# Kernel optimization log

Measured on AMD Instinct MI355X. Metric: run time of the kernel, lower is better.

The kernel has to match this reference:

```python
import jax, jax.numpy as jnp
import numpy as np

LAGRANGE_ORDER = 5  # fixed, as in the torch module


def _lagrange_weights(alpha):
    """Vectorised Lagrange weights of length L+1. alpha: [B,N] -> [B,N,L+1]."""
    L = LAGRANGE_ORDER
    j = jnp.arange(L + 1, dtype=alpha.dtype)
    u = alpha[..., None] - j                          # [B,N,L+1]
    denom = j[:, None] - j[None, :]                   # [L+1,L+1]
    mask = ~jnp.eye(L + 1, dtype=bool)
    num = jnp.where(mask, u[..., None, :], jnp.ones_like(u)[..., None, :])
    den = jnp.where(mask, denom, jnp.ones_like(denom))
    return (num / den).prod(axis=-1)                  # [B,N,L+1]


def setup_inputs() -> dict:
    key = jax.random.key(0)
    k1, k2, k3 = jax.random.split(key, 3)
    B, N = 16, 16384
    # fractional period in samples, in [40, 100) -> max floor(f0)=99, K=99+5+3=107<=108
    f0 = 40.0 + 60.0 * jax.random.uniform(k1, (B, N), dtype=jnp.float32)
    x = jax.random.normal(k2, (B, N), dtype=jnp.float32)
    l_b = jax.random.uniform(k3, (B, N, 2), dtype=jnp.float32)  # (g, p) in [0,1]
    return {"f0": f0, "x": x, "l_b": l_b, "K": 108}


def reference(f0, x, l_b, K):
    B, N = x.shape
    L = LAGRANGE_ORDER
    # design_loop: (g, p) -> loop taps [b0, a1]; gain capped <1 for stability
    g = 0.99 * l_b[..., 0]
    p = l_b[..., 1]
    b0 = g * (1.0 - p)                                # [B,N]
    a1 = g * p
    # tune_f0: subtract low-frequency phase delay of (b0 + a1 z^-1)
    f0c = f0 - a1 / (b0 + a1 + 1e-7)
    # Lagrange centre & weights
    z = jnp.floor(f0c).astype(jnp.int32)
    z_center = z - L // 2                             # [B,N]
    alpha = f0c - z_center.astype(f0.dtype)
    w = _lagrange_weights(alpha)                      # [B,N,L+1]
    # compute_resonator_matrix: loop filter convolved with fractional delay -> block [B,N,L+2]
    block = (b0[..., None] * jnp.pad(w, ((0, 0), (0, 0), (0, 1)))
             + a1[..., None] * jnp.pad(w, ((0, 0), (0, 0), (1, 0))))
    # scatter (-block) into A; LPC lag k+1 lives in column k
    cols = z_center[..., None] - 1 + jnp.arange(L + 2)  # [B,N,L+2]
    cols = jnp.clip(cols, 0, K - 1)
    A = jnp.zeros((B, N, K), x.dtype).at[
        jnp.arange(B)[:, None, None], jnp.arange(N)[None, :, None], cols
    ].add(-block)
    # sample_wise_lpc: y[n] = x[n] - sum_k A[n,k] * y[n-1-k], zero init state
    def step(buf, inp):
        a_n, x_n = inp                                 # [B,K], [B]
        y_n = x_n - jnp.sum(a_n * buf, axis=-1)
        buf = jnp.concatenate([y_n[:, None], buf[:, :-1]], axis=1)
        return buf, y_n
    buf0 = jnp.zeros((B, K), x.dtype)
    _, ys = jax.lax.scan(step, buf0, (A.transpose(1, 0, 2), x.T))  # ys: [N,B]
    return ys.T
```

## Files before the change

### kernel.cpp

```cpp
#include <hip/hip_runtime.h>
#include <math.h>


#define B_    16
#define N_    16384
#define S_    16
#define NSEG  1024
#define NITER 28
#define RUNS  104
#define CHUNK 37
#define HROWS 263
#define ZROW0 150

#define TG_FLOATS (B_ * S_ * RUNS * RUNS)
#define ST_FLOATS (B_ * S_ * RUNS)

__device__ __forceinline__ void diffks_coeffs(float f0v, float lbg, float lbp,
                                              int n, float4& lo, float4& hi) {
  float g  = 0.99f * lbg;
  float p  = lbp;
  float b0 = g * (1.0f - p);
  float a1 = g * p;
  float f0c = f0v - a1 / (b0 + a1 + 1e-7f);
  int   zc  = (int)floorf(f0c) - 2;
  float alpha = f0c - (float)zc;
  float u0 = alpha;
  float u1 = alpha - 1.0f;
  float u2 = alpha - 2.0f;
  float u3 = alpha - 3.0f;
  float u4 = alpha - 4.0f;
  float u5 = alpha - 5.0f;
  float w0 = u1 * u2 * u3 * u4 * u5 * (-1.0f / 120.0f);
  float w1 = u0 * u2 * u3 * u4 * u5 * ( 1.0f /  24.0f);
  float w2 = u0 * u1 * u3 * u4 * u5 * (-1.0f /  12.0f);
  float w3 = u0 * u1 * u2 * u4 * u5 * ( 1.0f /  12.0f);
  float w4 = u0 * u1 * u2 * u3 * u5 * (-1.0f /  24.0f);
  float w5 = u0 * u1 * u2 * u3 * u4 * ( 1.0f / 120.0f);
  lo.x = b0 * w0;
  lo.y = fmaf(b0, w1, a1 * w0);
  lo.z = fmaf(b0, w2, a1 * w1);
  lo.w = fmaf(b0, w3, a1 * w2);
  hi.x = fmaf(b0, w4, a1 * w3);
  hi.y = fmaf(b0, w5, a1 * w4);
  hi.z = a1 * w5;
  hi.w = __int_as_float((n - 6 - zc) & 255);
}

__global__ __launch_bounds__(1024) void diffks_phase1(
    const float* __restrict__ f0, const float* __restrict__ lb,
    const float* __restrict__ x, float* __restrict__ Tg) {
  const int bs = blockIdx.x;
  const int b  = bs >> 4, s = bs & 15;
  const int n0 = s << 10;
  const int tid = threadIdx.x;

  __shared__ __align__(16) float hist[HROWS * RUNS];
  __shared__ float4 sLo[NSEG], sHi[NSEG];
  __shared__ float  sX[NSEG];

  {
    const size_t gi = (size_t)b * N_ + n0 + tid;
    const float2 lv = ((const float2*)lb)[gi];
    float4 lo, hi;
    diffks_coeffs(f0[gi], lv.x, lv.y, tid, lo, hi);
    sLo[tid] = lo; sHi[tid] = hi; sX[tid] = x[gi];
  }
  {
    float4* __restrict__ hz = (float4*)(hist + ZROW0 * RUNS);
    const int nz = ((HROWS - ZROW0) * RUNS) / 4;
    for (int i = tid; i < nz; i += 1024)
      hz[i] = float4{0.0f, 0.0f, 0.0f, 0.0f};
  }
  __syncthreads();
  if (tid < 103) hist[(255 - tid) * RUNS + tid] = 1.0f;
  __syncthreads();

  {
    const int w    = tid >> 6;
    const int lane = tid & 63;
    const int cl   = 2 * lane;
    const bool act = (lane < 52);
    const bool px  = (lane == 51);
    float* __restrict__ hcol = hist + cl;

    for (int t = 0; t < 32; ++t) {
#pragma unroll
      for (int u = 0; u < 2; ++u) {
        const int p = 32 * t + 2 * w + u;
        const float4 lo = sLo[p];
        const float4 hi = sHi[p];
        const float  xv = sX[p];
        if (act) {
          const int base = __float_as_int(hi.w);
          const float* __restrict__ hr = hcol + base * RUNS;
          float2 acc;
          acc.x = 0.0f;
          acc.y = px ? xv : 0.0f;
          const float c[7] = {hi.z, hi.y, hi.x, lo.w, lo.z, lo.y, lo.x};
#pragma unroll
          for (int m = 0; m < 7; ++m) {
            const float2 v = *(const float2*)(hr + m * RUNS);
            acc.x = fmaf(c[m], v.x, acc.x);
            acc.y = fmaf(c[m], v.y, acc.y);
          }
          const int wsl = p & 255;
          *(float2*)(hcol + wsl * RUNS) = acc;
          if (wsl < 7)
            *(float2*)(hcol + (wsl + 256) * RUNS) = acc;
        }
      }
      __syncthreads();
    }
  }

  float* __restrict__ T = Tg + (size_t)bs * RUNS * RUNS;
  for (int idx = tid; idx < RUNS * RUNS; idx += 1024) {
    const int r = idx / RUNS;
    const int j = idx - r * RUNS;
    T[idx] = (j < 103) ? hist[((255 - j) & 255) * RUNS + r] : 0.0f;
  }
}

#define P2_STEP(s_, tv_)                                                      \
  {                                                                           \
    if (q == 0) states[((size_t)b * S_ + (s_)) * RUNS + j] = cur[j];          \
    float acc = 0.0f;                                                         \
    _Pragma("unroll")                                                         \
    for (int k = 0; k < 13; ++k) acc = fmaf(tv_[k], cur[r0 + k], acc);        \
    if ((s_) + 2 < S_) {                                                      \
      const float* __restrict__ Tn = Tb + (size_t)((s_) + 2) * RUNS * RUNS;   \
      _Pragma("unroll")                                                       \
      for (int k = 0; k < 13; ++k) tv_[k] = Tn[(size_t)(r0 + k) * RUNS + j];  \
    }                                                                         \
    part[q][j] = acc;                                                         \
    __syncthreads();                                                          \
    if (q == 0) {                                                             \
      float v = 0.0f;                                                         \
      _Pragma("unroll")                                                       \
      for (int qq = 0; qq < 8; ++qq) v += part[qq][j];                        \
      cur[j] = (j < 103) ? v : 1.0f;                                          \
    }                                                                         \
    __syncthreads();                                                          \
  }

__global__ __launch_bounds__(832) void diffks_phase2(
    const float* __restrict__ Tg, float* __restrict__ states) {
  const int b   = blockIdx.x;
  const int tid = threadIdx.x;
  const int j   = tid % RUNS;
  const int q   = tid / RUNS;
  const int r0  = 13 * q;
  __shared__ float cur[RUNS];
  __shared__ float part[8][105];
  if (tid < 103) cur[tid] = 0.0f;
  if (tid == 103) cur[103] = 1.0f;
  __syncthreads();

  const float* __restrict__ Tb = Tg + (size_t)b * S_ * RUNS * RUNS;
  float tvA[13], tvB[13];
#pragma unroll
  for (int k = 0; k < 13; ++k)
    tvA[k] = Tb[(size_t)(r0 + k) * RUNS + j];
#pragma unroll
  for (int k = 0; k < 13; ++k)
    tvB[k] = Tb[(size_t)RUNS * RUNS + (size_t)(r0 + k) * RUNS + j];

#pragma unroll
  for (int sp = 0; sp < 8; ++sp) {
    P2_STEP(2 * sp,     tvA)
    P2_STEP(2 * sp + 1, tvB)
  }
}

__global__ __launch_bounds__(256) void diffks_phase3(
    const float* __restrict__ f0, const float* __restrict__ lb,
    const float* __restrict__ x, const float* __restrict__ states,
    float* __restrict__ y) {
  const int bs = blockIdx.x;
  const int b  = bs >> 4, s = bs & 15;
  const int n0 = s << 10;
  const int tid = threadIdx.x;

  __shared__ __align__(16) float ring[512];
  __shared__ float4 sC[2 * NSEG];
  __shared__ float  sX[NSEG];
  __shared__ float  sY[NSEG];

#pragma unroll
  for (int k = 0; k < 2; ++k) ring[tid + 256 * k] = 0.0f;
  {
    const size_t gb = (size_t)b * N_ + n0;
    const float*  __restrict__ f0b = f0 + gb;
    const float2* __restrict__ lbb = (const float2*)(lb + 2 * gb);
    const float*  __restrict__ xb  = x + gb;
    float  vf[4]; float2 vl[4]; float vx[4];
#pragma unroll
    for (int k = 0; k < 4; ++k) {
      const int i = tid + 256 * k;
      vf[k] = f0b[i]; vl[k] = lbb[i]; vx[k] = xb[i];
    }
#pragma unroll
    for (int k = 0; k < 4; ++k) {
      const int i = tid + 256 * k;
      float4 lo, hi;
      diffks_coeffs(vf[k], vl[k].x, vl[k].y, n0 + i, lo, hi);
      sC[2 * i] = lo; sC[2 * i + 1] = hi; sX[i] = vx[k];
    }
  }
  __syncthreads();
  const float* __restrict__ st = states + (size_t)bs * RUNS;
  if (tid < 103) {
    const float v = st[tid];
    ring[255 - tid] = v;
    ring[511 - tid] = v;
  }
  __syncthreads();

  if (tid < 64) {
    const int lane = tid;
    const bool act = (lane < CHUNK);
    for (int t = 0; t < NITER; ++t) {
      const int p = t * CHUNK + lane;
      if (act && p < NSEG) {
        const float4 lo = sC[2 * p];
        const float4 hi = sC[2 * p + 1];
        const float  xv = sX[p];
        const int base = __float_as_int(hi.w);
        const float r0 = ring[base + 0];
        const float r1 = ring[base + 1];
        const float r2 = ring[base + 2];
        const float r3 = ring[base + 3];
        const float r4 = ring[base + 4];
        const float r5 = ring[base + 5];
        const float r6 = ring[base + 6];
        const float s0 = fmaf(lo.x, r6, xv);
        const float s1 = fmaf(lo.y, r5, lo.z * r4);
        const float s2 = fmaf(lo.w, r3, hi.x * r2);
        const float s3 = fmaf(hi.y, r1, hi.z * r0);
        const float yv = (s0 + s1) + (s2 + s3);
        const int wsl = p & 255;
        ring[wsl]       = yv;
        ring[wsl + 256] = yv;
        sY[p] = yv;
      }
      __builtin_amdgcn_wave_barrier();
      asm volatile("" ::: "memory");
    }
  }
  __syncthreads();

  float4* __restrict__ yb = (float4*)(y + (size_t)b * N_ + n0);
  yb[tid] = ((const float4*)sY)[tid];
}

__global__ __launch_bounds__(256) void diffks_coeff_fb(
    const float* __restrict__ f0, const float* __restrict__ lb,
    float* __restrict__ cw, int total, int Nmask) {
  int idx = blockIdx.x * blockDim.x + threadIdx.x;
  if (idx >= total) return;
  float4 lo, hi;
  diffks_coeffs(f0[idx], lb[2 * idx], lb[2 * idx + 1], idx & Nmask, lo, hi);
  float4* out4 = (float4*)cw;
  out4[2 * idx]     = lo;
  out4[2 * idx + 1] = hi;
}

__global__ __launch_bounds__(64) void diffks_scan_fb(
    const float* __restrict__ x, const float* __restrict__ cw,
    float* __restrict__ y, int N) {
  const int b    = blockIdx.x;
  const int lane = threadIdx.x;
  __shared__ float ring[512];
#pragma unroll
  for (int i = 0; i < 8; ++i) ring[lane + 64 * i] = 0.0f;
  __builtin_amdgcn_wave_barrier();
  asm volatile("" ::: "memory");
  const float4* __restrict__ c4 = (const float4*)(cw + (size_t)b * N * 8);
  const float*  __restrict__ xb = x + (size_t)b * N;
  float*        __restrict__ yb = y + (size_t)b * N;
  const bool act = (lane < CHUNK);
  const int nIter = (N + CHUNK - 1) / CHUNK;
  for (int t = 0; t < nIter; ++t) {
    const int n = t * CHUNK + lane;
    if (act && n < N) {
      const float4 lo = c4[2 * n];
      const float4 hi = c4[2 * n + 1];
      const float  xv = xb[n];
      const int base = __float_as_int(hi.w);
      const float r0 = ring[base + 0];
      const float r1 = ring[base + 1];
      const float r2 = ring[base + 2];
      const float r3 = ring[base + 3];
      const float r4 = ring[base + 4];
      const float r5 = ring[base + 5];
      const float r6 = ring[base + 6];
      const float s0 = fmaf(lo.x, r6, xv);
      const float s1 = fmaf(lo.y, r5, lo.z * r4);
      const float s2 = fmaf(lo.w, r3, hi.x * r2);
      const float s3 = fmaf(hi.y, r1, hi.z * r0);
      const float yv = (s0 + s1) + (s2 + s3);
      ring[n & 255]         = yv;
      ring[(n & 255) + 256] = yv;
      yb[n] = yv;
    }
    __builtin_amdgcn_wave_barrier();
    asm volatile("" ::: "memory");
  }
}

extern "C" void kernel_launch(void* const* d_in, const int* in_sizes, int n_in,
                              void* d_out, int out_size, void* d_ws, size_t ws_size,
                              hipStream_t stream) {
  const float* f0 = (const float*)d_in[0];
  const float* x  = (const float*)d_in[1];
  const float* lb = (const float*)d_in[2];
  float* out = (float*)d_out;

  const int total = in_sizes[0];
  const size_t need = (size_t)(TG_FLOATS + ST_FLOATS) * 4;

  if (total == B_ * N_ && ws_size >= need) {
    float* Tg = (float*)d_ws;
    float* st = Tg + TG_FLOATS;
    diffks_phase1<<<B_ * S_, 1024, 0, stream>>>(f0, lb, x, Tg);
    diffks_phase2<<<B_, 832, 0, stream>>>(Tg, st);
    diffks_phase3<<<B_ * S_, 256, 0, stream>>>(f0, lb, x, st, out);
  } else {
    const int N = total / B_;
    float* cw = (float*)d_ws;
    diffks_coeff_fb<<<(total + 255) / 256, 256, 0, stream>>>(f0, lb, cw, total, N - 1);
    diffks_scan_fb<<<B_, 64, 0, stream>>>(x, cw, out, N);
  }
}
```

Before: 108.1 us.

## Broadcast per-step coefficients via readlane and process two steps per wave with float4

Phase 1 no longer stages the per-sample coefficients in shared-memory arrays. Each lane computes the coefficients for one of the wave's assigned samples and holds them in registers, and every step broadcasts them with readlane. Each wave now splits its lanes into two halves that handle the two interleaved samples at once, with each lane covering 4 columns via float4 LDS accesses instead of 2 via float2. This removes the LDS coefficient reads and halves the inner iterations per sync, at the cost of many readlane/select instructions and more complex wrap-row write conditions.

Result: no change. 108.5 us (+0.4%).

```diff
diff --git a/kernel.cpp b/kernel.cpp
--- a/kernel.cpp
+++ b/kernel.cpp
@@ -10,10 +10,11 @@
 #define RUNS  104
 #define CHUNK 37
 #define HROWS 263
-#define ZROW0 150
 
 #define TG_FLOATS (B_ * S_ * RUNS * RUNS)
 #define ST_FLOATS (B_ * S_ * RUNS)
+
+#define RL(v, l) __int_as_float(__builtin_amdgcn_readlane(__float_as_int(v), (l)))
 
 __device__ __forceinline__ void diffks_coeffs(float f0v, float lbg, float lbp,
                                               int n, float4& lo, float4& hi) {
@@ -53,21 +54,23 @@
   const int b  = bs >> 4, s = bs & 15;
   const int n0 = s << 10;
   const int tid = threadIdx.x;
+  const int w    = tid >> 6;
+  const int lane = tid & 63;
 
   __shared__ __align__(16) float hist[HROWS * RUNS];
-  __shared__ float4 sLo[NSEG], sHi[NSEG];
-  __shared__ float  sX[NSEG];
-
+
+  float4 cLo, cHi; float cX;
   {
-    const size_t gi = (size_t)b * N_ + n0 + tid;
+    const int my_p = 32 * (lane & 31) + 2 * w + (lane >> 5);
+    const size_t gi = (size_t)b * N_ + n0 + my_p;
     const float2 lv = ((const float2*)lb)[gi];
-    float4 lo, hi;
-    diffks_coeffs(f0[gi], lv.x, lv.y, tid, lo, hi);
-    sLo[tid] = lo; sHi[tid] = hi; sX[tid] = x[gi];
-  }
+    diffks_coeffs(f0[gi], lv.x, lv.y, my_p, cLo, cHi);
+    cX = x[gi];
+  }
+
   {
-    float4* __restrict__ hz = (float4*)(hist + ZROW0 * RUNS);
-    const int nz = ((HROWS - ZROW0) * RUNS) / 4;
+    float4* __restrict__ hz = (float4*)(hist + 152 * RUNS);
+    const int nz = ((HROWS - 152) * RUNS) / 4;
     for (int i = tid; i < nz; i += 1024)
       hz[i] = float4{0.0f, 0.0f, 0.0f, 0.0f};
   }
@@ -76,38 +79,48 @@
   __syncthreads();
 
   {
-    const int w    = tid >> 6;
-    const int lane = tid & 63;
-    const int cl   = 2 * lane;
-    const bool act = (lane < 52);
-    const bool px  = (lane == 51);
-    float* __restrict__ hcol = hist + cl;
+    const bool half = (lane >= 26);
+    const int  l4   = half ? lane - 26 : lane;
+    const bool act  = (lane < 52);
+    const bool px   = (l4 == 25);
+    float* __restrict__ hq = hist + 4 * l4;
 
     for (int t = 0; t < 32; ++t) {
-#pragma unroll
-      for (int u = 0; u < 2; ++u) {
-        const int p = 32 * t + 2 * w + u;
-        const float4 lo = sLo[p];
-        const float4 hi = sHi[p];
-        const float  xv = sX[p];
-        if (act) {
-          const int base = __float_as_int(hi.w);
-          const float* __restrict__ hr = hcol + base * RUNS;
-          float2 acc;
-          acc.x = 0.0f;
-          acc.y = px ? xv : 0.0f;
-          const float c[7] = {hi.z, hi.y, hi.x, lo.w, lo.z, lo.y, lo.x};
-#pragma unroll
-          for (int m = 0; m < 7; ++m) {
-            const float2 v = *(const float2*)(hr + m * RUNS);
-            acc.x = fmaf(c[m], v.x, acc.x);
-            acc.y = fmaf(c[m], v.y, acc.y);
-          }
-          const int wsl = p & 255;
-          *(float2*)(hcol + wsl * RUNS) = acc;
-          if (wsl < 7)
-            *(float2*)(hcol + (wsl + 256) * RUNS) = acc;
+      const int lA = t, lB = t + 32;
+      const float c0A = RL(cHi.z, lA), c0B = RL(cHi.z, lB);
+      const float c1A = RL(cHi.y, lA), c1B = RL(cHi.y, lB);
+      const float c2A = RL(cHi.x, lA), c2B = RL(cHi.x, lB);
+      const float c3A = RL(cLo.w, lA), c3B = RL(cLo.w, lB);
+      const float c4A = RL(cLo.z, lA), c4B = RL(cLo.z, lB);
+      const float c5A = RL(cLo.y, lA), c5B = RL(cLo.y, lB);
+      const float c6A = RL(cLo.x, lA), c6B = RL(cLo.x, lB);
+      const float bwA = RL(cHi.w, lA), bwB = RL(cHi.w, lB);
+      const float xA  = RL(cX,   lA), xB  = RL(cX,   lB);
+
+      if (act) {
+        const float c[7] = {half ? c0B : c0A, half ? c1B : c1A,
+                            half ? c2B : c2A, half ? c3B : c3A,
+                            half ? c4B : c4A, half ? c5B : c5A,
+                            half ? c6B : c6A};
+        const int   base = __float_as_int(half ? bwB : bwA);
+        const float xv   = half ? xB : xA;
+        const float4* __restrict__ hr = (const float4*)(hq + base * RUNS);
+        float4 a;
+        a.x = 0.0f; a.y = 0.0f; a.z = 0.0f;
+        a.w = px ? xv : 0.0f;
+#pragma unroll
+        for (int m = 0; m < 7; ++m) {
+          const float4 v = hr[m * 26];
+          a.x = fmaf(c[m], v.x, a.x);
+          a.y = fmaf(c[m], v.y, a.y);
+          a.z = fmaf(c[m], v.z, a.z);
+          a.w = fmaf(c[m], v.w, a.w);
         }
+        const int p   = 32 * t + 2 * w + (half ? 1 : 0);
+        const int wsl = p & 255;
+        *(float4*)(hq + wsl * RUNS) = a;
+        if (((t & 7) == 0) && (w < 4) && (wsl < 7))
+          *(float4*)(hq + (wsl + 256) * RUNS) = a;
       }
       __syncthreads();
     }
@@ -117,7 +130,7 @@
   for (int idx = tid; idx < RUNS * RUNS; idx += 1024) {
     const int r = idx / RUNS;
     const int j = idx - r * RUNS;
-    T[idx] = (j < 103) ? hist[((255 - j) & 255) * RUNS + r] : 0.0f;
+    T[idx] = (j < 103) ? hist[(255 - j) * RUNS + r] : 0.0f;
   }
 }
 
```
